# Kernel optimization log

Measured on AMD Instinct MI355X. Metric: run time of the kernel, lower is better.

Reference implementation:

```python
import jax, jax.numpy as jnp
import numpy as np

D_MODEL = 1024
N_HEADS = 16
HEAD_DIM = D_MODEL // N_HEADS
D_FF = 4 * D_MODEL
SEQ = 2048
BATCH = 2
EPS = 1e-6


def setup_inputs() -> dict:
    key = jax.random.key(0)
    ks = jax.random.split(key, 8)
    s = 0.02
    return {
        "x": jax.random.normal(ks[0], (SEQ, BATCH, D_MODEL), dtype=jnp.float32),
        "g1": jnp.ones((D_MODEL,), dtype=jnp.float32),                # norm1 weight
        "g2": jnp.ones((D_MODEL,), dtype=jnp.float32),                # norm2 weight
        "Wq": jax.random.normal(ks[1], (N_HEADS, D_MODEL, HEAD_DIM), dtype=jnp.float32) * s,
        "Wk": jax.random.normal(ks[2], (N_HEADS, D_MODEL, HEAD_DIM), dtype=jnp.float32) * s,
        "Wv": jax.random.normal(ks[3], (N_HEADS, D_MODEL, HEAD_DIM), dtype=jnp.float32) * s,
        "Wo": jax.random.normal(ks[4], (D_MODEL, D_MODEL), dtype=jnp.float32) * s,
        "W1": jax.random.normal(ks[5], (D_MODEL, D_FF), dtype=jnp.float32) * s,
        "W2": jax.random.normal(ks[6], (D_FF, D_MODEL), dtype=jnp.float32) * s,
    }


def _rmsnorm(x, g):
    rms = jnp.sqrt(jnp.mean(x * x, axis=-1, keepdims=True) + EPS)
    return g * (x / rms)


def _block(x, g1, g2, Wq, Wk, Wv, Wo, W1, W2):
    S = x.shape[0]
    scale = HEAD_DIM ** -0.5
    # --- attention (pre-norm) ---
    h = _rmsnorm(x, g1)                              # (S, B, D)
    Q = jnp.einsum('sbd,hdk->bhsk', h, Wq)           # (B, H, S, K)
    K = jnp.einsum('sbd,hdk->bhsk', h, Wk)
    V = jnp.einsum('sbd,hdk->bhsk', h, Wv)
    scores = jnp.einsum('bhsk,bhtk->bhst', Q, K) * scale
    causal = jnp.tril(jnp.ones((S, S), dtype=bool))
    scores = jnp.where(causal, scores, -jnp.inf)
    attn = jax.nn.softmax(scores, axis=-1)
    ctx = jnp.einsum('bhst,bhtk->sbhk', attn, V)     # heads concatenated in order
    ctx = ctx.reshape(S, x.shape[1], D_MODEL)
    x = x + ctx @ Wo
    # --- FFN (pre-norm) ---
    h2 = _rmsnorm(x, g2)
    x = x + jax.nn.silu(h2 @ W1) @ W2
    return x


def reference(x, g1, g2, Wq, Wk, Wv, Wo, W1, W2):
    return _block(x, g1, g2, Wq, Wk, Wv, Wo, W1, W2)
```

## Files before the change

### kernel.cpp

```cpp
#include <hip/hip_runtime.h>

typedef unsigned short u16;
typedef __bf16 bf16x8 __attribute__((ext_vector_type(8)));
typedef u16 u16x8 __attribute__((ext_vector_type(8)));
typedef u16 u16x4 __attribute__((ext_vector_type(4)));
typedef float f32x4 __attribute__((ext_vector_type(4)));

__device__ __forceinline__ u16 f2bf(float f) {
    union { float f; unsigned int u; } x; x.f = f;
    unsigned int r = x.u + 0x7FFFu + ((x.u >> 16) & 1u);
    return (u16)(r >> 16);
}

__device__ __forceinline__ u16 f2bf_hw(float f) {
    union { __bf16 b; u16 u; } x; x.b = (__bf16)f; return x.u;
}

__device__ __forceinline__ void gload_lds16(const u16* g, u16* l) {
    __builtin_amdgcn_global_load_lds(
        (const __attribute__((address_space(1))) unsigned int*)g,
        (__attribute__((address_space(3))) unsigned int*)l, 16, 0, 0);
}


__global__ __launch_bounds__(256) void qkvT_k(
    const float* __restrict__ Wq, const float* __restrict__ Wk,
    const float* __restrict__ Wv, u16* __restrict__ out)
{
    __shared__ float T[64][65];
    const int d0 = blockIdx.x * 64;
    const int y = blockIdx.y;
    const int wsel = y >> 4, h = y & 15;
    const float* W = (wsel == 0) ? Wq : (wsel == 1) ? Wk : Wv;
    const float scale = (wsel == 0) ? 0.125f * 1.44269504088896f : 1.0f;
    const int tid = threadIdx.x;
    const int tr = tid >> 4;
    const int tc = (tid & 15) * 4;
    #pragma unroll
    for (int k = 0; k < 4; k++) {
        f32x4 v = *(const f32x4*)(W + (size_t)h * 65536 + (size_t)(d0 + 16 * k + tr) * 64 + tc);
        T[16 * k + tr][tc]     = v[0];
        T[16 * k + tr][tc + 1] = v[1];
        T[16 * k + tr][tc + 2] = v[2];
        T[16 * k + tr][tc + 3] = v[3];
    }
    __syncthreads();
    #pragma unroll
    for (int k = 0; k < 4; k++) {
        const int kk = 16 * k + tr;
        u16x4 o;
        #pragma unroll
        for (int i = 0; i < 4; i++) o[i] = f2bf(T[tc + i][kk] * scale);
        *(u16x4*)(out + (size_t)(wsel * 1024 + h * 64 + kk) * 1024 + d0 + tc) = o;
    }
}

__global__ __launch_bounds__(256) void transT_k(
    const float* __restrict__ in, u16* __restrict__ out, int R, int C)
{
    __shared__ float T[64][65];
    const int r0 = blockIdx.x * 64, c0 = blockIdx.y * 64;
    const int tid = threadIdx.x;
    const int tr = tid >> 4;
    const int tc = (tid & 15) * 4;
    #pragma unroll
    for (int k = 0; k < 4; k++) {
        f32x4 v = *(const f32x4*)(in + (size_t)(c0 + 16 * k + tr) * R + r0 + tc);
        T[16 * k + tr][tc]     = v[0];
        T[16 * k + tr][tc + 1] = v[1];
        T[16 * k + tr][tc + 2] = v[2];
        T[16 * k + tr][tc + 3] = v[3];
    }
    __syncthreads();
    #pragma unroll
    for (int k = 0; k < 4; k++) {
        const int rl = 16 * k + tr;
        u16x4 o;
        #pragma unroll
        for (int i = 0; i < 4; i++) o[i] = f2bf(T[tc + i][rl]);
        *(u16x4*)(out + (size_t)(r0 + rl) * C + c0 + tc) = o;
    }
}

__global__ __launch_bounds__(256) void vtrans_k(const u16* __restrict__ qkv, u16* __restrict__ vT)
{
    __shared__ u16 T[64][72];
    const int bh = blockIdx.x, b = bh >> 4, h = bh & 15;
    const int s0 = blockIdx.y * 64;
    const int tid = threadIdx.x;
    const int r = tid >> 2, c0 = (tid & 3) * 16;
    const u16* src = qkv + ((size_t)((s0 + r) * 2 + b)) * 3072 + 2048 + h * 64 + c0;
    *(u16x8*)&T[r][c0] = *(const u16x8*)src;
    *(u16x8*)&T[r][c0 + 8] = *(const u16x8*)(src + 8);
    __syncthreads();
    u16x8 o0, o1;
    #pragma unroll
    for (int i = 0; i < 8; i++) o0[i] = T[c0 + i][r];
    #pragma unroll
    for (int i = 0; i < 8; i++) o1[i] = T[c0 + 8 + i][r];
    u16* dst = vT + (size_t)(bh * 64 + r) * 2048 + s0 + c0;
    *(u16x8*)dst = o0;
    *(u16x8*)(dst + 8) = o1;
}

__global__ __launch_bounds__(256) void rmsnorm_k(
    const float* __restrict__ x, const float* __restrict__ g, u16* __restrict__ out)
{
    const int row = blockIdx.x;
    const int tid = threadIdx.x;
    const float* xr = x + (size_t)row * 1024;
    f32x4 v = *(const f32x4*)(xr + tid * 4);
    float ss = v[0] * v[0] + v[1] * v[1] + v[2] * v[2] + v[3] * v[3];
    #pragma unroll
    for (int off = 32; off > 0; off >>= 1) ss += __shfl_down(ss, off);
    __shared__ float red[4];
    if ((tid & 63) == 0) red[tid >> 6] = ss;
    __syncthreads();
    float sum = red[0] + red[1] + red[2] + red[3];
    float rinv = rsqrtf(sum * (1.0f / 1024.0f) + 1e-6f);
    f32x4 gv = *(const f32x4*)(g + tid * 4);
    u16x4 o;
    #pragma unroll
    for (int i = 0; i < 4; i++) o[i] = f2bf(v[i] * gv[i] * rinv);
    *(u16x4*)(out + (size_t)row * 1024 + tid * 4) = o;
}

__global__ __launch_bounds__(256) void addred_norm_k(
    const float* __restrict__ res, const float* __restrict__ p0,
    const float* __restrict__ p1, const float* __restrict__ g,
    float* __restrict__ xout, u16* __restrict__ hout)
{
    const int row = blockIdx.x;
    const int tid = threadIdx.x;
    const size_t base = (size_t)row * 1024 + tid * 4;
    f32x4 a = *(const f32x4*)(res + base);
    f32x4 b = *(const f32x4*)(p0 + base);
    f32x4 c = *(const f32x4*)(p1 + base);
    f32x4 o = a + b + c;
    *(f32x4*)(xout + base) = o;
    float ss = o[0] * o[0] + o[1] * o[1] + o[2] * o[2] + o[3] * o[3];
    #pragma unroll
    for (int off = 32; off > 0; off >>= 1) ss += __shfl_down(ss, off);
    __shared__ float red[4];
    if ((tid & 63) == 0) red[tid >> 6] = ss;
    __syncthreads();
    float sum = red[0] + red[1] + red[2] + red[3];
    float rinv = rsqrtf(sum * (1.0f / 1024.0f) + 1e-6f);
    f32x4 gv = *(const f32x4*)(g + tid * 4);
    u16x4 hv;
    #pragma unroll
    for (int i = 0; i < 4; i++) hv[i] = f2bf(o[i] * gv[i] * rinv);
    *(u16x4*)(hout + base) = hv;
}

__global__ __launch_bounds__(256) void addred_k(
    const float* __restrict__ res, const float* __restrict__ p0,
    const float* __restrict__ p1, float* __restrict__ out)
{
    int i = (blockIdx.x * 256 + threadIdx.x) * 4;
    f32x4 a = *(const f32x4*)(res + i);
    f32x4 b = *(const f32x4*)(p0 + i);
    f32x4 c = *(const f32x4*)(p1 + i);
    f32x4 o = a + b + c;
    *(f32x4*)(out + i) = o;
}

template <int MODE>
__global__ __launch_bounds__(256) void gemm_bt_k(
    const u16* __restrict__ A, const u16* __restrict__ BT,
    u16* __restrict__ outB, float* __restrict__ outF, const float* __restrict__ res,
    int M, int N, int K, int klen)
{
    __shared__ u16 As[2][128 * 64];
    __shared__ u16 Bs[2][128 * 64];
    const int tid = threadIdx.x;
    const int lane = tid & 63, w = tid >> 6;
    const int wm = w >> 1, wn = w & 1;
    const int quad = lane >> 4, l15 = lane & 15;
    const int bid = blockIdx.x + gridDim.x * blockIdx.y;
    const int bj = bid >> 3;
    const int m0 = ((bid & 7) * 4 + (bj & 3)) * 128;
    const int n0 = (bj >> 2) * 128;
    const int kbeg = blockIdx.z * klen;

    f32x4 acc[4][4] = {};

    const int srow = (w << 3) + (lane >> 3);
    const int swz = ((lane & 7) ^ (lane >> 3)) << 3;
    const u16* aA = A + (size_t)(m0 + srow) * K + kbeg + swz;
    const u16* aB = BT + (size_t)(n0 + srow) * K + kbeg + swz;
    const int wo = w * 512;
    const int rsw = (l15 & 7) << 3;

    #pragma unroll
    for (int c = 0; c < 4; c++) {
        gload_lds16(aA + (size_t)(c * 32) * K, &As[0][0] + c * 2048 + wo);
        gload_lds16(aB + (size_t)(c * 32) * K, &Bs[0][0] + c * 2048 + wo);
    }

    int cur = 0;
    for (int k0 = 0; k0 < klen; k0 += 64) {
        __syncthreads();
        if (k0 + 64 < klen) {
            #pragma unroll
            for (int c = 0; c < 4; c++) {
                gload_lds16(aA + (size_t)(c * 32) * K + k0 + 64, &As[cur ^ 1][0] + c * 2048 + wo);
                gload_lds16(aB + (size_t)(c * 32) * K + k0 + 64, &Bs[cur ^ 1][0] + c * 2048 + wo);
            }
        }
        const u16* AB = &As[cur][0];
        const u16* BB = &Bs[cur][0];
        #pragma unroll
        for (int kh = 0; kh < 2; kh++) {
            const int cb = ((kh * 4 + quad) << 3);
            bf16x8 af[4], bfr[4];
            #pragma unroll
            for (int i = 0; i < 4; i++)
                af[i] = *(const bf16x8*)(AB + (wm * 64 + i * 16 + l15) * 64 + (cb ^ rsw));
            #pragma unroll
            for (int j = 0; j < 4; j++)
                bfr[j] = *(const bf16x8*)(BB + (wn * 64 + j * 16 + l15) * 64 + (cb ^ rsw));
            #pragma unroll
            for (int i = 0; i < 4; i++)
                #pragma unroll
                for (int j = 0; j < 4; j++)
                    acc[i][j] = __builtin_amdgcn_mfma_f32_16x16x32_bf16(af[i], bfr[j], acc[i][j], 0, 0, 0);
        }
        cur ^= 1;
    }

    float* outFz = (MODE == 3) ? outF + (size_t)blockIdx.z * M * N : outF;
    #pragma unroll
    for (int i = 0; i < 4; i++) {
        const int row = m0 + wm * 64 + i * 16 + quad * 4;
        #pragma unroll
        for (int j = 0; j < 4; j++) {
            const int col = n0 + wn * 64 + j * 16 + l15;
            #pragma unroll
            for (int r = 0; r < 4; r++) {
                const size_t idx = (size_t)(row + r) * N + col;
                float v = acc[i][j][r];
                if (MODE == 0) {
                    outB[idx] = f2bf_hw(v);
                } else if (MODE == 1) {
                    outF[idx] = res[idx] + v;
                } else if (MODE == 2) {
                    float e = exp2f(v * -1.44269504088896f);
                    outB[idx] = f2bf_hw(v * __builtin_amdgcn_rcpf(1.0f + e));
                } else {
                    outFz[idx] = v;
                }
            }
        }
    }
}

__global__ __launch_bounds__(256) void attn_k(const u16* __restrict__ qkv,
                                              const u16* __restrict__ vT,
                                              u16* __restrict__ ctx)
{
    const int bh = blockIdx.x;
    const int qt = 31 - (int)blockIdx.y;
    const int b = bh >> 4, h = bh & 15;
    const int q0 = qt * 64;
    const int tid = threadIdx.x;
    const int lane = tid & 63, w = tid >> 6;
    const int quad = lane >> 4, l15 = lane & 15;

    __shared__ u16 QP[64][72];
    __shared__ u16 Ks[2][4096];
    __shared__ u16 Vs[2][4096];

    {
        const int r = tid >> 2, c0 = (tid & 3) * 16;
        const u16* src = qkv + ((size_t)((q0 + r) * 2 + b)) * 3072 + h * 64 + c0;
        *(u16x8*)&QP[r][c0] = *(const u16x8*)(src);
        *(u16x8*)&QP[r][c0 + 8] = *(const u16x8*)(src + 8);
    }
    __syncthreads();

    const bf16x8 aq0 = *(const bf16x8*)&QP[16 * w + l15][quad * 8];
    const bf16x8 aq1 = *(const bf16x8*)&QP[16 * w + l15][32 + quad * 8];

    bf16x8 ones;
    #pragma unroll
    for (int i = 0; i < 8; i++) ones[i] = (__bf16)1.0f;

    const int kr = (w << 3) + (lane >> 3);
    const int swz = ((lane & 7) ^ (lane >> 3)) << 3;
    const int ldsoff = w * 512;
    const u16* kbase0 = qkv + ((size_t)(kr * 2 + b)) * 3072 + 1024 + h * 64 + swz;
    const u16* kbase1 = kbase0 + (size_t)32 * 2 * 3072;
    const u16* vrow0 = vT + (size_t)(bh * 64 + kr) * 2048 + swz;
    const u16* vrow1 = vrow0 + (size_t)32 * 2048;

    const int rsw = (l15 & 7) << 3;

    f32x4 o[4] = {};
    f32x4 accl = {};

    gload_lds16(kbase0, &Ks[0][0] + ldsoff);
    gload_lds16(kbase1, &Ks[0][0] + 2048 + ldsoff);
    gload_lds16(vrow0, &Vs[0][0] + ldsoff);
    gload_lds16(vrow1, &Vs[0][0] + 2048 + ldsoff);

    int cur = 0;
    for (int t0 = 0; t0 <= q0; t0 += 64) {
        __syncthreads();
        if (t0 + 64 <= q0) {
            const size_t go = (size_t)(t0 + 64) * 2 * 3072;
            u16* KB = &Ks[cur ^ 1][0];
            u16* VB = &Vs[cur ^ 1][0];
            gload_lds16(kbase0 + go, KB + ldsoff);
            gload_lds16(kbase1 + go, KB + 2048 + ldsoff);
            gload_lds16(vrow0 + (t0 + 64), VB + ldsoff);
            gload_lds16(vrow1 + (t0 + 64), VB + 2048 + ldsoff);
        }
        const u16* KB = &Ks[cur][0];
        const u16* VB = &Vs[cur][0];

        f32x4 s[4];
        #pragma unroll
        for (int j = 0; j < 4; j++) {
            const u16* kb = KB + (j * 16 + l15) * 64;
            bf16x8 bk0 = *(const bf16x8*)(kb + (((quad << 3) ^ rsw)));
            bf16x8 bk1 = *(const bf16x8*)(kb + ((((quad + 4) << 3) ^ rsw)));
            f32x4 c = {};
            c = __builtin_amdgcn_mfma_f32_16x16x32_bf16(aq0, bk0, c, 0, 0, 0);
            c = __builtin_amdgcn_mfma_f32_16x16x32_bf16(aq1, bk1, c, 0, 0, 0);
            s[j] = c;
        }

        if (t0 == q0) {
            #pragma unroll
            for (int j = 0; j < 4; j++)
                #pragma unroll
                for (int r = 0; r < 4; r++)
                    if ((j * 16 + l15) > (16 * w + quad * 4 + r)) s[j][r] = -1e30f;
        }

        #pragma unroll
        for (int j = 0; j < 4; j++)
            #pragma unroll
            for (int r = 0; r < 4; r++)
                QP[16 * w + quad * 4 + r][j * 16 + l15] = f2bf_hw(exp2f(s[j][r]));

        bf16x8 ap0 = *(const bf16x8*)&QP[16 * w + l15][quad * 8];
        bf16x8 ap1 = *(const bf16x8*)&QP[16 * w + l15][32 + quad * 8];
        accl = __builtin_amdgcn_mfma_f32_16x16x32_bf16(ap0, ones, accl, 0, 0, 0);
        accl = __builtin_amdgcn_mfma_f32_16x16x32_bf16(ap1, ones, accl, 0, 0, 0);
        #pragma unroll
        for (int j = 0; j < 4; j++) {
            const u16* vb = VB + (j * 16 + l15) * 64;
            bf16x8 bv0 = *(const bf16x8*)(vb + (((quad << 3) ^ rsw)));
            bf16x8 bv1 = *(const bf16x8*)(vb + ((((quad + 4) << 3) ^ rsw)));
            o[j] = __builtin_amdgcn_mfma_f32_16x16x32_bf16(ap0, bv0, o[j], 0, 0, 0);
            o[j] = __builtin_amdgcn_mfma_f32_16x16x32_bf16(ap1, bv1, o[j], 0, 0, 0);
        }
        cur ^= 1;
    }

    f32x4 linv;
    #pragma unroll
    for (int r = 0; r < 4; r++) linv[r] = 1.0f / accl[r];
    #pragma unroll
    for (int j = 0; j < 4; j++)
        #pragma unroll
        for (int r = 0; r < 4; r++) {
            int q = q0 + 16 * w + quad * 4 + r;
            int col = h * 64 + j * 16 + l15;
            ctx[((size_t)q * 2 + b) * 1024 + col] = f2bf_hw(o[j][r] * linv[r]);
        }
}

extern "C" void kernel_launch(void* const* d_in, const int* in_sizes, int n_in,
                              void* d_out, int out_size, void* d_ws, size_t ws_size,
                              hipStream_t stream)
{
    (void)in_sizes; (void)n_in; (void)out_size; (void)ws_size;
    const float* x  = (const float*)d_in[0];
    const float* g1 = (const float*)d_in[1];
    const float* g2 = (const float*)d_in[2];
    const float* Wq = (const float*)d_in[3];
    const float* Wk = (const float*)d_in[4];
    const float* Wv = (const float*)d_in[5];
    const float* Wo = (const float*)d_in[6];
    const float* W1 = (const float*)d_in[7];
    const float* W2 = (const float*)d_in[8];
    float* out = (float*)d_out;

    char* ws = (char*)d_ws;
    u16*   bqkvT = (u16*)(ws);
    u16*   woT   = (u16*)(ws + 6291456);
    u16*   w1T   = (u16*)(ws + 8388608);
    u16*   w2T   = (u16*)(ws + 16777216);
    u16*   h1    = (u16*)(ws + 25165824);
    u16*   qkvB  = (u16*)(ws + 33554432);
    u16*   ctxB  = (u16*)(ws + 58720256);
    float* xmid  = (float*)(ws + 67108864);
    u16*   h2    = (u16*)(ws + 83886080);
    u16*   actB  = (u16*)(ws + 92274688);
    u16*   vT    = (u16*)(ws + 25165824);
    float* part  = (float*)(ws + 25165824);
    float* partO = (float*)(ws + 92274688);

    qkvT_k<<<dim3(16, 48), 256, 0, stream>>>(Wq, Wk, Wv, bqkvT);
    transT_k<<<dim3(16, 16), 256, 0, stream>>>(Wo, woT, 1024, 1024);
    transT_k<<<dim3(64, 16), 256, 0, stream>>>(W1, w1T, 4096, 1024);
    transT_k<<<dim3(16, 64), 256, 0, stream>>>(W2, w2T, 1024, 4096);

    rmsnorm_k<<<4096, 256, 0, stream>>>(x, g1, h1);

    gemm_bt_k<0><<<dim3(24, 32), 256, 0, stream>>>(h1, bqkvT, qkvB, nullptr, nullptr,
                                                   4096, 3072, 1024, 1024);
    vtrans_k<<<dim3(32, 32), 256, 0, stream>>>(qkvB, vT);
    attn_k<<<dim3(32, 32), 256, 0, stream>>>(qkvB, vT, ctxB);

    gemm_bt_k<3><<<dim3(8, 32, 2), 256, 0, stream>>>(ctxB, woT, nullptr, partO, nullptr,
                                                     4096, 1024, 1024, 512);
    addred_norm_k<<<4096, 256, 0, stream>>>(x, partO, partO + 4096 * 1024, g2, xmid, h2);

    gemm_bt_k<2><<<dim3(32, 32), 256, 0, stream>>>(h2, w1T, actB, nullptr, nullptr,
                                                   4096, 4096, 1024, 1024);
    gemm_bt_k<3><<<dim3(8, 32, 2), 256, 0, stream>>>(actB, w2T, nullptr, part, nullptr,
                                                     4096, 1024, 4096, 2048);
    addred_k<<<4096 * 1024 / 1024, 256, 0, stream>>>(xmid, part, part + 4096 * 1024, out);
}
```

Measured before the change: 331.9 us.

## Add 256x256-tile 8-wave pipelined GEMM for QKV, FFN1 and FFN2

Adds a new GEMM kernel that uses 256x256 output tiles with 8 waves, a ping-pong staging schedule that splits each K step into halves, XOR-swizzled LDS, and raised priority around the MFMA blocks. The QKV, W1+SiLU and W2 GEMMs move onto it, and W2 now uses a 4-way split-K whose partials are summed by a new addred4 kernel. Workspace buffers are remapped so xmid and the four partial buffers do not collide. The larger tiles are meant to raise data reuse and MFMA utilisation. The costs are more partial-sum traffic and fewer workgroups per GEMM, so the grids are smaller.

```diff
diff --git a/kernel.cpp b/kernel.cpp
--- a/kernel.cpp
+++ b/kernel.cpp
@@ -153,16 +153,18 @@
     *(u16x4*)(hout + base) = hv;
 }
 
-__global__ __launch_bounds__(256) void addred_k(
-    const float* __restrict__ res, const float* __restrict__ p0,
-    const float* __restrict__ p1, float* __restrict__ out)
+__global__ __launch_bounds__(256) void addred4_k(
+    const float* __restrict__ xm, const float* __restrict__ a0,
+    const float* __restrict__ a1, const float* __restrict__ a2,
+    const float* __restrict__ a3, float* __restrict__ out)
 {
     int i = (blockIdx.x * 256 + threadIdx.x) * 4;
-    f32x4 a = *(const f32x4*)(res + i);
-    f32x4 b = *(const f32x4*)(p0 + i);
-    f32x4 c = *(const f32x4*)(p1 + i);
-    f32x4 o = a + b + c;
-    *(f32x4*)(out + i) = o;
+    f32x4 v = *(const f32x4*)(xm + i);
+    v = v + *(const f32x4*)(a0 + i);
+    v = v + *(const f32x4*)(a1 + i);
+    v = v + *(const f32x4*)(a2 + i);
+    v = v + *(const f32x4*)(a3 + i);
+    *(f32x4*)(out + i) = v;
 }
 
 template <int MODE>
@@ -255,6 +257,157 @@
     }
 }
 
+#define MM8(FH) \
+    { _Pragma("unroll") \
+      for (int i_ = 0; i_ < 4; i_++) { \
+        acc[(FH)*4+i_][0] = __builtin_amdgcn_mfma_f32_16x16x32_bf16(a[i_], b0, acc[(FH)*4+i_][0], 0, 0, 0); \
+        acc[(FH)*4+i_][1] = __builtin_amdgcn_mfma_f32_16x16x32_bf16(a[i_], b1, acc[(FH)*4+i_][1], 0, 0, 0); \
+        acc[(FH)*4+i_][2] = __builtin_amdgcn_mfma_f32_16x16x32_bf16(a[i_], b2, acc[(FH)*4+i_][2], 0, 0, 0); \
+        acc[(FH)*4+i_][3] = __builtin_amdgcn_mfma_f32_16x16x32_bf16(a[i_], b3, acc[(FH)*4+i_][3], 0, 0, 0); \
+      } }
+
+template <int MODE>
+__global__ __launch_bounds__(512, 2) void gemm8p_k(
+    const u16* __restrict__ A, const u16* __restrict__ BT,
+    u16* __restrict__ outB, float* __restrict__ q0, float* __restrict__ q1,
+    float* __restrict__ q2, float* __restrict__ q3,
+    int N, int K, int klen)
+{
+    __shared__ u16 sm[65536];
+    const int tid = threadIdx.x;
+    const int lane = tid & 63, w = tid >> 6;
+    const int l15 = lane & 15, quad = lane >> 4;
+    const int wm = w >> 2, wn = w & 3;
+
+    const int nwg = gridDim.x;
+    const int bid = blockIdx.x;
+    const int s = (bid & 7) * (nwg >> 3) + (bid >> 3);
+    const int m0 = (s & 15) * 256;
+    const int n0 = (s >> 4) * 256;
+    const int kbeg = blockIdx.z * klen;
+    const int nT = klen >> 6;
+
+    const int srow = w * 16 + (lane >> 2);
+    const int scol = (((lane & 3) ^ ((lane >> 3) & 3)) << 3);
+    const u16* gA = A + (size_t)(m0 + srow) * K + kbeg + scol;
+    const u16* gB = BT + (size_t)(n0 + srow) * K + kbeg + scol;
+    const size_t cstep = (size_t)128 * K;
+
+    const int rswz = ((quad ^ ((l15 >> 1) & 3)) << 3);
+    const int raoff = (wm * 128 + l15) * 32 + rswz;
+    const int rboff = (wn * 64 + l15) * 32 + rswz;
+
+    f32x4 acc[8][4] = {};
+
+    auto stA = [&](int t, int kh) {
+        u16* d = sm + (t & 1) * 32768 + kh * 8192 + w * 512;
+        const u16* g = gA + (size_t)(t * 64 + kh * 32);
+        gload_lds16(g, d);
+        gload_lds16(g + cstep, d + 4096);
+    };
+    auto stB = [&](int t, int kh) {
+        u16* d = sm + (t & 1) * 32768 + 16384 + kh * 8192 + w * 512;
+        const u16* g = gB + (size_t)(t * 64 + kh * 32);
+        gload_lds16(g, d);
+        gload_lds16(g + cstep, d + 4096);
+    };
+    bf16x8 b0, b1, b2, b3;
+    auto rdB = [&](int buf, int kh) {
+        const u16* p = sm + buf * 32768 + 16384 + kh * 8192 + rboff;
+        b0 = *(const bf16x8*)(p);
+        b1 = *(const bf16x8*)(p + 512);
+        b2 = *(const bf16x8*)(p + 1024);
+        b3 = *(const bf16x8*)(p + 1536);
+    };
+    auto rdA = [&](int buf, int kh, int fh, bf16x8* a) {
+        const u16* p = sm + buf * 32768 + kh * 8192 + fh * 2048 + raoff;
+        a[0] = *(const bf16x8*)(p);
+        a[1] = *(const bf16x8*)(p + 512);
+        a[2] = *(const bf16x8*)(p + 1024);
+        a[3] = *(const bf16x8*)(p + 1536);
+    };
+
+    stA(0, 0); stB(0, 0); stA(0, 1); stB(0, 1);
+    if (nT > 1) {
+        stA(1, 0); stB(1, 0);
+        asm volatile("s_waitcnt vmcnt(4)" ::: "memory");
+    } else {
+        asm volatile("s_waitcnt vmcnt(0)" ::: "memory");
+    }
+    __builtin_amdgcn_s_barrier();
+
+    for (int t = 0; t < nT; t++) {
+        const int buf = t & 1;
+        bf16x8 a[4];
+        rdA(buf, 0, 0, a); rdB(buf, 0);
+        if (t + 1 < nT) stA(t + 1, 1);
+        __builtin_amdgcn_s_barrier();
+        asm volatile("s_waitcnt lgkmcnt(0)" ::: "memory");
+        __builtin_amdgcn_sched_barrier(0);
+        __builtin_amdgcn_s_setprio(1);
+        MM8(0)
+        __builtin_amdgcn_s_setprio(0);
+        __builtin_amdgcn_s_barrier();
+        rdA(buf, 0, 1, a);
+        if (t + 1 < nT) stB(t + 1, 1);
+        __builtin_amdgcn_s_barrier();
+        asm volatile("s_waitcnt lgkmcnt(0)" ::: "memory");
+        __builtin_amdgcn_sched_barrier(0);
+        __builtin_amdgcn_s_setprio(1);
+        MM8(1)
+        __builtin_amdgcn_s_setprio(0);
+        __builtin_amdgcn_s_barrier();
+        rdA(buf, 1, 0, a); rdB(buf, 1);
+        if (t + 2 < nT) stA(t + 2, 0);
+        __builtin_amdgcn_s_barrier();
+        asm volatile("s_waitcnt lgkmcnt(0)" ::: "memory");
+        __builtin_amdgcn_sched_barrier(0);
+        __builtin_amdgcn_s_setprio(1);
+        MM8(0)
+        __builtin_amdgcn_s_setprio(0);
+        __builtin_amdgcn_s_barrier();
+        rdA(buf, 1, 1, a);
+        if (t + 2 < nT) {
+            stB(t + 2, 0);
+            asm volatile("s_waitcnt vmcnt(4)" ::: "memory");
+        } else {
+            asm volatile("s_waitcnt vmcnt(0)" ::: "memory");
+        }
+        __builtin_amdgcn_s_barrier();
+        asm volatile("s_waitcnt lgkmcnt(0)" ::: "memory");
+        __builtin_amdgcn_sched_barrier(0);
+        __builtin_amdgcn_s_setprio(1);
+        MM8(1)
+        __builtin_amdgcn_s_setprio(0);
+        __builtin_amdgcn_s_barrier();
+    }
+
+    float* po = nullptr;
+    if (MODE == 3)
+        po = (blockIdx.z == 0) ? q0 : (blockIdx.z == 1) ? q1 : (blockIdx.z == 2) ? q2 : q3;
+    #pragma unroll
+    for (int mf = 0; mf < 8; mf++) {
+        const int row = m0 + wm * 128 + mf * 16 + quad * 4;
+        #pragma unroll
+        for (int nf = 0; nf < 4; nf++) {
+            const int col = n0 + wn * 64 + nf * 16 + l15;
+            #pragma unroll
+            for (int r = 0; r < 4; r++) {
+                const size_t idx = (size_t)(row + r) * N + col;
+                const float v = acc[mf][nf][r];
+                if (MODE == 0) {
+                    outB[idx] = f2bf_hw(v);
+                } else if (MODE == 2) {
+                    float e = exp2f(v * -1.44269504088896f);
+                    outB[idx] = f2bf_hw(v * __builtin_amdgcn_rcpf(1.0f + e));
+                } else {
+                    po[idx] = v;
+                }
+            }
+        }
+    }
+}
+
 __global__ __launch_bounds__(256) void attn_k(const u16* __restrict__ qkv,
                                               const u16* __restrict__ vT,
                                               u16* __restrict__ ctx)
@@ -396,13 +549,16 @@
     u16*   w2T   = (u16*)(ws + 16777216);
     u16*   h1    = (u16*)(ws + 25165824);
     u16*   qkvB  = (u16*)(ws + 33554432);
+    u16*   vT    = (u16*)(ws + 25165824);
     u16*   ctxB  = (u16*)(ws + 58720256);
-    float* xmid  = (float*)(ws + 67108864);
+    float* xmid  = (float*)(ws + 41943040);
     u16*   h2    = (u16*)(ws + 83886080);
     u16*   actB  = (u16*)(ws + 92274688);
-    u16*   vT    = (u16*)(ws + 25165824);
-    float* part  = (float*)(ws + 25165824);
     float* partO = (float*)(ws + 92274688);
+    float* p0 = (float*)(ws);
+    float* p1 = (float*)(ws + 25165824);
+    float* p2 = (float*)(ws + 58720256);
+    float* p3 = (float*)(ws + 75497472);
 
     qkvT_k<<<dim3(16, 48), 256, 0, stream>>>(Wq, Wk, Wv, bqkvT);
     transT_k<<<dim3(16, 16), 256, 0, stream>>>(Wo, woT, 1024, 1024);
@@ -411,8 +567,9 @@
 
     rmsnorm_k<<<4096, 256, 0, stream>>>(x, g1, h1);
 
-    gemm_bt_k<0><<<dim3(24, 32), 256, 0, stream>>>(h1, bqkvT, qkvB, nullptr, nullptr,
-                                                   4096, 3072, 1024, 1024);
+    gemm8p_k<0><<<dim3(192, 1, 1), 512, 0, stream>>>(h1, bqkvT, qkvB,
+                                                     nullptr, nullptr, nullptr, nullptr,
+                                                     3072, 1024, 1024);
     vtrans_k<<<dim3(32, 32), 256, 0, stream>>>(qkvB, vT);
     attn_k<<<dim3(32, 32), 256, 0, stream>>>(qkvB, vT, ctxB);
 
@@ -420,9 +577,11 @@
                                                      4096, 1024, 1024, 512);
     addred_norm_k<<<4096, 256, 0, stream>>>(x, partO, partO + 4096 * 1024, g2, xmid, h2);
 
-    gemm_bt_k<2><<<dim3(32, 32), 256, 0, stream>>>(h2, w1T, actB, nullptr, nullptr,
-                                                   4096, 4096, 1024, 1024);
-    gemm_bt_k<3><<<dim3(8, 32, 2), 256, 0, stream>>>(actB, w2T, nullptr, part, nullptr,
-                                                     4096, 1024, 4096, 2048);
-    addred_k<<<4096 * 1024 / 1024, 256, 0, stream>>>(xmid, part, part + 4096 * 1024, out);
-}
+    gemm8p_k<2><<<dim3(256, 1, 1), 512, 0, stream>>>(h2, w1T, actB,
+                                                     nullptr, nullptr, nullptr, nullptr,
+                                                     4096, 1024, 1024);
+    gemm8p_k<3><<<dim3(64, 1, 4), 512, 0, stream>>>(actB, w2T, nullptr,
+                                                    p0, p1, p2, p3,
+                                                    1024, 4096, 1024);
+    addred4_k<<<4096 * 1024 / 1024, 256, 0, stream>>>(xmid, p0, p1, p2, p3, out);
+}
```

After: 330.7 us. About the same (-0.4%).
